# Kernel optimization log

Hardware: AMD Instinct MI355X
Metric: run time of the kernel (lower is better)

Reference implementation:

```python
import jax, jax.numpy as jnp
import numpy as np

D = 256
HEADS = 8
LEVELS = 4
POINTS = 4
HD = D // HEADS  # 32
SHAPES = [(96, 96), (48, 48), (24, 24), (12, 12)]
N_BATCH = 2


def setup_inputs() -> dict:
    key = jax.random.key(0)
    ks = jax.random.split(key, 10)
    Lin = sum(h * w for h, w in SHAPES)  # 12240
    src = jax.random.normal(ks[0], (N_BATCH, Lin, D), jnp.float32)
    reference_points = jax.random.uniform(ks[1], (N_BATCH, Lin, LEVELS, 2), jnp.float32)
    spatial_shapes = np.array(SHAPES, dtype=np.int64)
    level_start_index = np.concatenate([[0], np.cumsum([h * w for h, w in SHAPES])[:-1]]).astype(np.int64)
    s = 0.02
    w_value = s * jax.random.normal(ks[2], (D, D), jnp.float32)
    b_value = jnp.zeros((D,), jnp.float32)
    w_off = s * jax.random.normal(ks[3], (D, HEADS * LEVELS * POINTS * 2), jnp.float32)
    b_off = 0.5 * jax.random.normal(ks[4], (HEADS * LEVELS * POINTS * 2,), jnp.float32)
    w_attn = s * jax.random.normal(ks[5], (D, HEADS * LEVELS * POINTS), jnp.float32)
    b_attn = jnp.zeros((HEADS * LEVELS * POINTS,), jnp.float32)
    w_out = s * jax.random.normal(ks[6], (D, D), jnp.float32)
    b_out = jnp.zeros((D,), jnp.float32)
    gamma = jnp.ones((D,), jnp.float32)
    beta = jnp.zeros((D,), jnp.float32)
    return dict(src=src, reference_points=reference_points, spatial_shapes=spatial_shapes,
                level_start_index=level_start_index, w_value=w_value, b_value=b_value,
                w_off=w_off, b_off=b_off, w_attn=w_attn, b_attn=b_attn,
                w_out=w_out, b_out=b_out, gamma=gamma, beta=beta)


def _bilinear_sample(value_flat, H, W, loc):
    # value_flat: (N, heads, H*W, hd); loc: (N, heads, Lq, P, 2) normalized [0,1]
    # Equivalent to F.grid_sample(bilinear, padding_mode='zeros', align_corners=False)
    x = loc[..., 0] * W - 0.5
    y = loc[..., 1] * H - 0.5
    x0 = jnp.floor(x)
    y0 = jnp.floor(y)
    lx = x - x0
    ly = y - y0
    n, h, Lq, P = x.shape
    out = jnp.zeros((n, h, Lq, P, value_flat.shape[-1]), value_flat.dtype)
    for dy, wy in ((0, 1.0 - ly), (1, ly)):
        for dx, wx in ((0, 1.0 - lx), (1, lx)):
            xi = x0 + dx
            yi = y0 + dy
            valid = (xi >= 0) & (xi < W) & (yi >= 0) & (yi < H)
            idx = (jnp.clip(yi, 0, H - 1) * W + jnp.clip(xi, 0, W - 1)).astype(jnp.int32)
            v = jnp.take_along_axis(value_flat, idx.reshape(n, h, Lq * P, 1), axis=2)
            v = v.reshape(n, h, Lq, P, -1)
            out = out + v * (wx * wy * valid.astype(value_flat.dtype))[..., None]
    return out


def reference(src, reference_points, spatial_shapes, level_start_index,
              w_value, b_value, w_off, b_off, w_attn, b_attn, w_out, b_out, gamma, beta):
    N, Lq, _ = src.shape
    shapes = np.asarray(spatial_shapes)
    starts = np.asarray(level_start_index)

    # projections
    value = (src @ w_value + b_value).reshape(N, Lq, HEADS, HD)
    offsets = (src @ w_off + b_off).reshape(N, Lq, HEADS, LEVELS, POINTS, 2)
    attn = (src @ w_attn + b_attn).reshape(N, Lq, HEADS, LEVELS * POINTS)
    attn = jax.nn.softmax(attn, axis=-1).reshape(N, Lq, HEADS, LEVELS, POINTS)

    # sampling locations: ref + offset / (W_l, H_l)
    normalizer = jnp.asarray(shapes[:, ::-1].copy(), jnp.float32)  # (L, 2) = (W, H)
    loc = reference_points[:, :, None, :, None, :] + offsets / normalizer[None, None, None, :, None, :]

    out = jnp.zeros((N, HEADS, Lq, HD), src.dtype)
    for l in range(LEVELS):
        H, W = int(shapes[l, 0]), int(shapes[l, 1])
        s0 = int(starts[l])
        v_l = value[:, s0:s0 + H * W].transpose(0, 2, 1, 3)        # (N, heads, HW, hd)
        loc_l = loc[:, :, :, l].transpose(0, 2, 1, 3, 4)           # (N, heads, Lq, P, 2)
        sampled = _bilinear_sample(v_l, H, W, loc_l)               # (N, heads, Lq, P, hd)
        w_l = attn[:, :, :, l].transpose(0, 2, 1, 3)               # (N, heads, Lq, P)
        out = out + (sampled * w_l[..., None]).sum(axis=3)
    out = out.transpose(0, 2, 1, 3).reshape(N, Lq, D)
    out = out @ w_out + b_out

    # residual (dropout in eval = identity) + LayerNorm
    x = src + out
    mu = x.mean(-1, keepdims=True)
    var = x.var(-1, keepdims=True)
    return (x - mu) / jnp.sqrt(var + 1e-5) * gamma + beta
```

## Files before the change

kernel.cpp:

```cpp
#include <hip/hip_runtime.h>
#include <cstdint>
#include <cstddef>

#define D 256
#define HEADS 8
#define HD 32
#define NB 2
#define LQ 12240
#define NQ (NB * LQ)
#define PLANE (LQ * HD)

typedef __attribute__((ext_vector_type(8))) short bf16x8;
typedef __attribute__((ext_vector_type(4))) float f32x4;
typedef __bf16 bf16x2 __attribute__((ext_vector_type(2)));

__device__ __forceinline__ ushort f2bf(float f) {
    union { float f; uint32_t u; } c; c.f = f;
    uint32_t u = c.u;
    uint32_t r = (u + 0x7fffu + ((u >> 16) & 1u)) >> 16;
    return (ushort)r;
}
__device__ __forceinline__ float bflo(uint32_t u) { return __uint_as_float(u << 16); }
__device__ __forceinline__ float bfhi(uint32_t u) { return __uint_as_float(u & 0xffff0000u); }

__device__ __forceinline__ float dot2bf(uint32_t a, uint32_t b, float c) {
#if __has_builtin(__builtin_amdgcn_fdot2_f32_bf16)
    return __builtin_amdgcn_fdot2_f32_bf16(__builtin_bit_cast(bf16x2, a),
                                           __builtin_bit_cast(bf16x2, b), c, false);
#else
    return c + bflo(a) * bflo(b) + bfhi(a) * bfhi(b);
#endif
}

__global__ __launch_bounds__(256) void conv_kernel(
    const float* __restrict__ w_value, const float* __restrict__ w_off,
    const float* __restrict__ w_attn,  const float* __restrict__ b_value,
    const float* __restrict__ b_off,   const float* __restrict__ b_attn,
    const float* __restrict__ w_out,   const float* __restrict__ src,
    ushort* __restrict__ B_pack, ushort* __restrict__ w_out_t,
    float* __restrict__ b_pack, ushort* __restrict__ src_bf)
{
    const int b = blockIdx.x, k = threadIdx.x;
    if (b >= 899) {
        const size_t i = ((size_t)(b - 899) * 256 + k) * 4;
        float4 v = *(const float4*)(src + i);
        ushort4 o;
        o.x = f2bf(v.x); o.y = f2bf(v.y); o.z = f2bf(v.z); o.w = f2bf(v.w);
        *(ushort4*)(src_bf + i) = o;
        return;
    }
    if (b < 640) {
        float v;
        if (b < 256)      v = w_value[(size_t)k * 256 + b];
        else if (b < 512) v = w_off[(size_t)k * 256 + (b - 256)];
        else              v = w_attn[(size_t)k * 128 + (b - 512)];
        B_pack[(size_t)b * 256 + k] = f2bf(v);
    } else if (b < 896) {
        int n = b - 640;
        w_out_t[(size_t)n * 256 + k] = f2bf(w_out[(size_t)k * 256 + n]);
    } else if (b == 896) {
        b_pack[k] = b_value[k];
    } else if (b == 897) {
        b_pack[256 + k] = b_off[k];
    } else {
        if (k < 128) b_pack[512 + k] = b_attn[k];
    }
}

__global__ __launch_bounds__(256, 2) void proj_gemm(
    const ushort* __restrict__ src_bf, const ushort* __restrict__ B_pack,
    const float* __restrict__ b_pack,
    ushort* __restrict__ val_t, float* __restrict__ off_raw,
    float* __restrict__ attn_raw)
{
    const int tid = threadIdx.x;
    const int wv = tid >> 6, lane = tid & 63;
    const int quad = lane >> 4, ln = lane & 15;
    const int mc = blockIdx.x;
    const int by = blockIdx.y;

    const ushort* bp = B_pack + (size_t)(by * 64 + ln) * 256 + quad * 8;
    bf16x8 bfr[4][8];
#pragma unroll
    for (int t = 0; t < 4; ++t)
#pragma unroll
        for (int s = 0; s < 8; ++s)
            bfr[t][s] = *(const bf16x8*)(bp + (size_t)t * (16 * 256) + s * 32);

    float bias[4];
#pragma unroll
    for (int t = 0; t < 4; ++t) bias[t] = b_pack[by * 64 + t * 16 + ln];

    for (int i = 0; i < 3; ++i) {
        const int base = (mc * 3 + i) * 64;
        if (base >= NQ) break;
        const int row_a = base + wv * 16 + ln;
        const bool va = row_a < NQ;
        const ushort* ap = src_bf + (size_t)row_a * 256 + quad * 8;

        bf16x8 af[8];
#pragma unroll
        for (int s = 0; s < 8; ++s) {
            bf16x8 v = {0, 0, 0, 0, 0, 0, 0, 0};
            if (va) v = *(const bf16x8*)(ap + s * 32);
            af[s] = v;
        }

        f32x4 acc[4] = {{0,0,0,0},{0,0,0,0},{0,0,0,0},{0,0,0,0}};
#pragma unroll
        for (int s = 0; s < 8; ++s)
#pragma unroll
            for (int t = 0; t < 4; ++t)
                acc[t] = __builtin_amdgcn_mfma_f32_16x16x32_bf16(af[s], bfr[t][s], acc[t], 0, 0, 0);

        if (by < 4) {
#pragma unroll
            for (int t = 0; t < 4; ++t) {
                const int n_g = by * 64 + t * 16 + ln;
                const int h = n_g >> 5, hd = n_g & 31;
#pragma unroll
                for (int reg = 0; reg < 4; ++reg) {
                    int row = base + wv * 16 + quad * 4 + reg;
                    if (row < NQ) {
                        int nb = row >= LQ; int ql = row - nb * LQ;
                        val_t[(((size_t)(nb * 8 + h)) * LQ + ql) * 32 + hd] =
                            f2bf(acc[t][reg] + bias[t]);
                    }
                }
            }
        } else if (by < 8) {
#pragma unroll
            for (int t = 0; t < 4; ++t) {
                const int col = (by - 4) * 64 + t * 16 + ln;
#pragma unroll
                for (int reg = 0; reg < 4; ++reg) {
                    int row = base + wv * 16 + quad * 4 + reg;
                    if (row < NQ)
                        off_raw[(size_t)row * 256 + col] = acc[t][reg] + bias[t];
                }
            }
        } else {
#pragma unroll
            for (int t = 0; t < 4; ++t) {
                const int col = (by - 8) * 64 + t * 16 + ln;
#pragma unroll
                for (int reg = 0; reg < 4; ++reg) {
                    int row = base + wv * 16 + quad * 4 + reg;
                    if (row < NQ)
                        attn_raw[(size_t)row * 128 + col] = acc[t][reg] + bias[t];
                }
            }
        }
    }
}

__global__ __launch_bounds__(256) void pair_kernel(
    const ushort* __restrict__ val_t, uint32_t* __restrict__ val_pair)
{
    const uint32_t j = blockIdx.x * 256 + threadIdx.x;
    const uint32_t c4 = (j & 7u) * 4u;
    const uint32_t rest = j >> 3;
    const uint32_t plane = rest / LQ;
    const uint32_t pos = rest - plane * LQ;
    int l = (pos >= 9216) + (pos >= 11520) + (pos >= 12096);
    uint32_t s0 = (l > 0 ? 9216u : 0u) + (l > 1 ? 2304u : 0u) + (l > 2 ? 576u : 0u);
    uint32_t Wi = 96u >> l;
    uint32_t p = pos - s0;
    uint32_t q = (p / 3u) >> (5 - l);
    uint32_t xr = p - q * Wi;
    uint32_t nxt = (xr == Wi - 1u) ? pos : pos + 1u;
    const ushort* base = val_t + (size_t)plane * PLANE;
    uint2 lo = *(const uint2*)(base + pos * 32 + c4);
    uint2 hi = *(const uint2*)(base + nxt * 32 + c4);
    uint4 o;
    o.x = (lo.x & 0x0000ffffu) | (hi.x << 16);
    o.y = (lo.x >> 16)         | (hi.x & 0xffff0000u);
    o.z = (lo.y & 0x0000ffffu) | (hi.y << 16);
    o.w = (lo.y >> 16)         | (hi.y & 0xffff0000u);
    *(uint4*)(val_pair + ((size_t)rest * 32 + c4)) = o;
}

__global__ __launch_bounds__(256) void sample_kernel(
    const float* __restrict__ ref_pts,
    const uint32_t* __restrict__ val_pair,
    const float* __restrict__ off_raw,
    const float* attn_raw,
    uint32_t* sampled)
{
    __shared__ uint32_t sm_i[16][2][18];
    __shared__ uint32_t sm_w[16][2][18];
    const int gl = threadIdx.x >> 4;
    const int ln = threadIdx.x & 15;
    const int h     = blockIdx.x & 7;
    const int chunk = blockIdx.x >> 3;
    const int qg = chunk * 16 + gl;
    const int n  = (qg >= LQ) ? 1 : 0;
    const int l  = ln >> 2;

    float a = attn_raw[(size_t)qg * 128 + h * 16 + ln];
    float m = a;
#pragma unroll
    for (int s = 8; s; s >>= 1) m = fmaxf(m, __shfl_xor(m, s, 16));
    float e = __expf(a - m);
    float ssum = e;
#pragma unroll
    for (int s = 8; s; s >>= 1) ssum += __shfl_xor(ssum, s, 16);
    float aw = e * __builtin_amdgcn_rcpf(ssum);

    float ox = off_raw[(size_t)qg * 256 + h * 32 + ln * 2 + 0];
    float oy = off_raw[(size_t)qg * 256 + h * 32 + ln * 2 + 1];
    float rx = ref_pts[(qg * 4 + l) * 2 + 0];
    float ry = ref_pts[(qg * 4 + l) * 2 + 1];

    const int Wi = 96 >> l;
    const int Hi = Wi;
    const int s0 = (l > 0 ? 9216 : 0) + (l > 1 ? 2304 : 0) + (l > 2 ? 576 : 0);
    const float Wf = (float)Wi, Hf = (float)Hi;

    float x = fmaf(rx, Wf, ox) - 0.5f;
    float y = fmaf(ry, Hf, oy) - 0.5f;
    float x0f = floorf(x), y0f = floorf(y);
    float lx = x - x0f, ly = y - y0f;
    int x0 = (int)x0f, y0 = (int)y0f;

    float wy0 = (y0 >= 0 && y0 < Hi) ? (1.f - ly) : 0.f;
    float wy1 = (y0 + 1 >= 0 && y0 + 1 < Hi) ? ly : 0.f;
    int yc0 = min(max(y0, 0), Hi - 1);
    int yc1 = min(max(y0 + 1, 0), Hi - 1);
    float wl = (x0 >= 0 && x0 < Wi) ? (1.f - lx) : 0.f;
    float wh = (x0 + 1 >= 0 && x0 + 1 < Wi) ? lx : 0.f;
    float pl, ph;
    int xe;
    if (x0 < 0) { pl = wh; ph = 0.f; xe = x0 + 1; }
    else        { pl = wl; ph = wh;  xe = x0; }
    int xc = min(max(xe, 0), Wi - 1);
    pl *= aw; ph *= aw;

    sm_i[gl][0][ln] = (uint32_t)(s0 + yc0 * Wi + xc) * 32u;
    sm_i[gl][1][ln] = (uint32_t)(s0 + yc1 * Wi + xc) * 32u;
    sm_w[gl][0][ln] = ((uint32_t)f2bf(ph * wy0) << 16) | (uint32_t)f2bf(pl * wy0);
    sm_w[gl][1][ln] = ((uint32_t)f2bf(ph * wy1) << 16) | (uint32_t)f2bf(pl * wy1);

    const int half = ln >> 3;
    const int cb   = (ln & 7) * 4;
    const uint32_t* plane =
        val_pair + (size_t)(n * HEADS + h) * PLANE + cb;

    float a0 = 0.f, a1 = 0.f, a2 = 0.f, a3 = 0.f;
#pragma unroll
    for (int c = 0; c < 2; ++c) {
        uint4    rv[8];
        uint32_t wpk[8];
#pragma unroll
        for (int p = 0; p < 8; ++p) {
            uint32_t off = sm_i[gl][half][c * 8 + p];
            rv[p]  = *(const uint4*)(plane + off);
            wpk[p] = sm_w[gl][half][c * 8 + p];
        }
#pragma unroll
        for (int p = 0; p < 8; ++p) {
            a0 = dot2bf(rv[p].x, wpk[p], a0);
            a1 = dot2bf(rv[p].y, wpk[p], a1);
            a2 = dot2bf(rv[p].z, wpk[p], a2);
            a3 = dot2bf(rv[p].w, wpk[p], a3);
        }
    }
    a0 += __shfl_xor(a0, 8, 16);
    a1 += __shfl_xor(a1, 8, 16);
    a2 += __shfl_xor(a2, 8, 16);
    a3 += __shfl_xor(a3, 8, 16);
    if (ln < 8) {
        uint2 rr;
        rr.x = ((uint32_t)f2bf(a1) << 16) | (uint32_t)f2bf(a0);
        rr.y = ((uint32_t)f2bf(a3) << 16) | (uint32_t)f2bf(a2);
        *(uint2*)(sampled + (size_t)qg * 128 + h * 16 + 2 * ln) = rr;
    }
}

__global__ __launch_bounds__(256, 2) void out_ln_gemm(
    const ushort* __restrict__ sampled, const ushort* __restrict__ w_out_t,
    const float* __restrict__ b_out,    const float* __restrict__ src,
    const float* __restrict__ gamma,    const float* __restrict__ beta,
    float* __restrict__ out)
{
    __shared__ float sm[2][4][16][2];
    const int tid = threadIdx.x;
    const int wv = tid >> 6, lane = tid & 63;
    const int quad = lane >> 4, ln = lane & 15;

    const ushort* bp = w_out_t + (size_t)(wv * 64 + ln) * 256 + quad * 8;
    bf16x8 bfr[4][8];
#pragma unroll
    for (int t = 0; t < 4; ++t)
#pragma unroll
        for (int s = 0; s < 8; ++s)
            bfr[t][s] = *(const bf16x8*)(bp + (size_t)t * (16 * 256) + s * 32);

    float bias[4], gam[4], bet[4];
#pragma unroll
    for (int t = 0; t < 4; ++t) {
        const int col = wv * 64 + t * 16 + ln;
        bias[t] = b_out[col];
        gam[t]  = gamma[col];
        bet[t]  = beta[col];
    }

    int base = blockIdx.x * 48;

    bf16x8 af[8];
    {
        const ushort* ap = sampled + (size_t)(base + ln) * 256 + quad * 8;
#pragma unroll
        for (int s = 0; s < 8; ++s) af[s] = *(const bf16x8*)(ap + s * 32);
    }

    for (int i = 0; i < 3; ++i) {
        bf16x8 afn[8];
        if (i < 2) {
            const ushort* apn = sampled + (size_t)(base + 16 + ln) * 256 + quad * 8;
#pragma unroll
            for (int s = 0; s < 8; ++s) afn[s] = *(const bf16x8*)(apn + s * 32);
        }
        float sv[4][4];
#pragma unroll
        for (int reg = 0; reg < 4; ++reg) {
            const float* sp = src + (size_t)(base + quad * 4 + reg) * 256 + wv * 64 + ln;
#pragma unroll
            for (int t = 0; t < 4; ++t) sv[reg][t] = sp[t * 16];
        }

        f32x4 acc[4] = {{0,0,0,0},{0,0,0,0},{0,0,0,0},{0,0,0,0}};
#pragma unroll
        for (int s = 0; s < 8; ++s)
#pragma unroll
            for (int t = 0; t < 4; ++t)
                acc[t] = __builtin_amdgcn_mfma_f32_16x16x32_bf16(af[s], bfr[t][s], acc[t], 0, 0, 0);

#pragma unroll
        for (int reg = 0; reg < 4; ++reg) {
            float s1 = 0.f, s2 = 0.f;
#pragma unroll
            for (int t = 0; t < 4; ++t) {
                float v = acc[t][reg] + bias[t] + sv[reg][t];
                acc[t][reg] = v;
                s1 += v; s2 += v * v;
            }
#pragma unroll
            for (int o = 8; o; o >>= 1) {
                s1 += __shfl_xor(s1, o, 16);
                s2 += __shfl_xor(s2, o, 16);
            }
            if (ln == 0) {
                sm[i & 1][wv][quad * 4 + reg][0] = s1;
                sm[i & 1][wv][quad * 4 + reg][1] = s2;
            }
        }
        __syncthreads();

#pragma unroll
        for (int reg = 0; reg < 4; ++reg) {
            const int r16 = quad * 4 + reg;
            float s1 = sm[i & 1][0][r16][0] + sm[i & 1][1][r16][0]
                     + sm[i & 1][2][r16][0] + sm[i & 1][3][r16][0];
            float s2 = sm[i & 1][0][r16][1] + sm[i & 1][1][r16][1]
                     + sm[i & 1][2][r16][1] + sm[i & 1][3][r16][1];
            float mu  = s1 * (1.f / 256.f);
            float var = s2 * (1.f / 256.f) - mu * mu;
            float rs  = rsqrtf(var + 1e-5f);
            const int row = base + quad * 4 + reg;
            float* op = out + (size_t)row * 256 + wv * 64 + ln;
#pragma unroll
            for (int t = 0; t < 4; ++t)
                op[t * 16] = (acc[t][reg] - mu) * rs * gam[t] + bet[t];
        }

        base += 16;
#pragma unroll
        for (int s = 0; s < 8; ++s) af[s] = afn[s];
    }
}

extern "C" void kernel_launch(void* const* d_in, const int* in_sizes, int n_in,
                              void* d_out, int out_size, void* d_ws, size_t ws_size,
                              hipStream_t stream)
{
    const float* src     = (const float*)d_in[0];
    const float* refp    = (const float*)d_in[1];
    const float* w_value = (const float*)d_in[4];
    const float* b_value = (const float*)d_in[5];
    const float* w_off   = (const float*)d_in[6];
    const float* b_off   = (const float*)d_in[7];
    const float* w_attn  = (const float*)d_in[8];
    const float* b_attn  = (const float*)d_in[9];
    const float* w_out   = (const float*)d_in[10];
    const float* b_out   = (const float*)d_in[11];
    const float* gamma   = (const float*)d_in[12];
    const float* beta    = (const float*)d_in[13];

    char* ws = (char*)d_ws;
    ushort*   val_t    = (ushort*)  (ws);
    uint32_t* val_pair = (uint32_t*)(ws + 12533760);
    ushort*   src_bf   = (ushort*)  (ws + 12533760);
    float*    off_raw  = (float*)   (ws + 37601280);
    float*    attn_raw = (float*)   (ws + 62668800);
    uint32_t* sampled  = (uint32_t*)(ws + 62668800);
    ushort*   B_pack   = (ushort*)  (ws + 75202560);
    ushort*   w_out_t  = (ushort*)  (ws + 75530240);
    float*    b_pack   = (float*)   (ws + 75661312);
    float*    out      = (float*)d_out;

    conv_kernel<<<7019, 256, 0, stream>>>(w_value, w_off, w_attn, b_value, b_off,
                                          b_attn, w_out, src, B_pack, w_out_t,
                                          b_pack, src_bf);
    proj_gemm<<<dim3(128, 10), 256, 0, stream>>>(src_bf, B_pack, b_pack, val_t,
                                                 off_raw, attn_raw);
    pair_kernel<<<6120, 256, 0, stream>>>(val_t, val_pair);
    sample_kernel<<<12240, 256, 0, stream>>>(refp, val_pair, off_raw, attn_raw,
                                             sampled);
    out_ln_gemm<<<510, 256, 0, stream>>>((const ushort*)sampled, w_out_t,
                                         b_out, src, gamma, beta, out);
}
```

Baseline: 199.4 us.

## Stage B tile in LDS and give each wave a 64x64 output tile in proj_gemm

proj_gemm used to hold the whole 64-column B slice in registers and loop over three 64-row chunks, with each wave computing a 16x64 tile. Now each block stages the 64x256 B slice in padded shared memory, and each wave computes a 64x64 tile (4x4 MFMA accumulators) over 256 rows, streaming A in K chunks. The grid shrinks from 128 to 96 blocks along M. The goal is to free the large B register file for more accumulators and more A reuse per B fragment, at the cost of LDS reads and a barrier, and with fewer blocks for a 256-CU part.

```diff
diff --git a/kernel.cpp b/kernel.cpp
--- a/kernel.cpp
+++ b/kernel.cpp
@@ -73,83 +73,102 @@
     ushort* __restrict__ val_t, float* __restrict__ off_raw,
     float* __restrict__ attn_raw)
 {
+    __shared__ ushort blds[64 * 264];
     const int tid = threadIdx.x;
     const int wv = tid >> 6, lane = tid & 63;
     const int quad = lane >> 4, ln = lane & 15;
     const int mc = blockIdx.x;
     const int by = blockIdx.y;
 
-    const ushort* bp = B_pack + (size_t)(by * 64 + ln) * 256 + quad * 8;
-    bf16x8 bfr[4][8];
-#pragma unroll
-    for (int t = 0; t < 4; ++t)
-#pragma unroll
-        for (int s = 0; s < 8; ++s)
-            bfr[t][s] = *(const bf16x8*)(bp + (size_t)t * (16 * 256) + s * 32);
+#pragma unroll
+    for (int j = 0; j < 8; ++j) {
+        const int idx = j * 256 + tid;
+        const int row = idx >> 5, c16 = idx & 31;
+        *(uint4*)(blds + row * 264 + c16 * 8) =
+            *(const uint4*)(B_pack + (size_t)(by * 64 + row) * 256 + c16 * 8);
+    }
 
     float bias[4];
 #pragma unroll
     for (int t = 0; t < 4; ++t) bias[t] = b_pack[by * 64 + t * 16 + ln];
 
-    for (int i = 0; i < 3; ++i) {
-        const int base = (mc * 3 + i) * 64;
-        if (base >= NQ) break;
-        const int row_a = base + wv * 16 + ln;
-        const bool va = row_a < NQ;
-        const ushort* ap = src_bf + (size_t)row_a * 256 + quad * 8;
-
-        bf16x8 af[8];
-#pragma unroll
-        for (int s = 0; s < 8; ++s) {
+    const int rowbase = mc * 256 + wv * 64;
+    bool va[4];
+#pragma unroll
+    for (int rt = 0; rt < 4; ++rt) va[rt] = (rowbase + rt * 16 + ln) < NQ;
+
+    __syncthreads();
+
+    f32x4 acc[4][4];
+#pragma unroll
+    for (int rt = 0; rt < 4; ++rt)
+#pragma unroll
+        for (int t = 0; t < 4; ++t) acc[rt][t] = (f32x4){0.f, 0.f, 0.f, 0.f};
+
+#pragma unroll 2
+    for (int kc = 0; kc < 8; ++kc) {
+        bf16x8 af[4], bf[4];
+#pragma unroll
+        for (int rt = 0; rt < 4; ++rt) {
             bf16x8 v = {0, 0, 0, 0, 0, 0, 0, 0};
-            if (va) v = *(const bf16x8*)(ap + s * 32);
-            af[s] = v;
-        }
-
-        f32x4 acc[4] = {{0,0,0,0},{0,0,0,0},{0,0,0,0},{0,0,0,0}};
-#pragma unroll
-        for (int s = 0; s < 8; ++s)
+            if (va[rt])
+                v = *(const bf16x8*)(src_bf +
+                      (size_t)(rowbase + rt * 16 + ln) * 256 + kc * 32 + quad * 8);
+            af[rt] = v;
+        }
+#pragma unroll
+        for (int t = 0; t < 4; ++t)
+            bf[t] = *(const bf16x8*)(blds + (t * 16 + ln) * 264 + kc * 32 + quad * 8);
+#pragma unroll
+        for (int rt = 0; rt < 4; ++rt)
 #pragma unroll
             for (int t = 0; t < 4; ++t)
-                acc[t] = __builtin_amdgcn_mfma_f32_16x16x32_bf16(af[s], bfr[t][s], acc[t], 0, 0, 0);
-
-        if (by < 4) {
-#pragma unroll
-            for (int t = 0; t < 4; ++t) {
-                const int n_g = by * 64 + t * 16 + ln;
-                const int h = n_g >> 5, hd = n_g & 31;
+                acc[rt][t] = __builtin_amdgcn_mfma_f32_16x16x32_bf16(
+                                 af[rt], bf[t], acc[rt][t], 0, 0, 0);
+    }
+
+    if (by < 4) {
+#pragma unroll
+        for (int t = 0; t < 4; ++t) {
+            const int n_g = by * 64 + t * 16 + ln;
+            const int h = n_g >> 5, hd = n_g & 31;
+#pragma unroll
+            for (int rt = 0; rt < 4; ++rt)
 #pragma unroll
                 for (int reg = 0; reg < 4; ++reg) {
-                    int row = base + wv * 16 + quad * 4 + reg;
+                    const int row = rowbase + rt * 16 + quad * 4 + reg;
                     if (row < NQ) {
-                        int nb = row >= LQ; int ql = row - nb * LQ;
+                        const int nb = row >= LQ; const int ql = row - nb * LQ;
                         val_t[(((size_t)(nb * 8 + h)) * LQ + ql) * 32 + hd] =
-                            f2bf(acc[t][reg] + bias[t]);
+                            f2bf(acc[rt][t][reg] + bias[t]);
                     }
                 }
-            }
-        } else if (by < 8) {
-#pragma unroll
-            for (int t = 0; t < 4; ++t) {
-                const int col = (by - 4) * 64 + t * 16 + ln;
+        }
+    } else if (by < 8) {
+#pragma unroll
+        for (int t = 0; t < 4; ++t) {
+            const int col = (by - 4) * 64 + t * 16 + ln;
+#pragma unroll
+            for (int rt = 0; rt < 4; ++rt)
 #pragma unroll
                 for (int reg = 0; reg < 4; ++reg) {
-                    int row = base + wv * 16 + quad * 4 + reg;
+                    const int row = rowbase + rt * 16 + quad * 4 + reg;
                     if (row < NQ)
-                        off_raw[(size_t)row * 256 + col] = acc[t][reg] + bias[t];
+                        off_raw[(size_t)row * 256 + col] = acc[rt][t][reg] + bias[t];
                 }
-            }
-        } else {
-#pragma unroll
-            for (int t = 0; t < 4; ++t) {
-                const int col = (by - 8) * 64 + t * 16 + ln;
+        }
+    } else {
+#pragma unroll
+        for (int t = 0; t < 4; ++t) {
+            const int col = (by - 8) * 64 + t * 16 + ln;
+#pragma unroll
+            for (int rt = 0; rt < 4; ++rt)
 #pragma unroll
                 for (int reg = 0; reg < 4; ++reg) {
-                    int row = base + wv * 16 + quad * 4 + reg;
+                    const int row = rowbase + rt * 16 + quad * 4 + reg;
                     if (row < NQ)
-                        attn_raw[(size_t)row * 128 + col] = acc[t][reg] + bias[t];
+                        attn_raw[(size_t)row * 128 + col] = acc[rt][t][reg] + bias[t];
                 }
-            }
         }
     }
 }
@@ -412,8 +431,8 @@
     conv_kernel<<<7019, 256, 0, stream>>>(w_value, w_off, w_attn, b_value, b_off,
                                           b_attn, w_out, src, B_pack, w_out_t,
                                           b_pack, src_bf);
-    proj_gemm<<<dim3(128, 10), 256, 0, stream>>>(src_bf, B_pack, b_pack, val_t,
-                                                 off_raw, attn_raw);
+    proj_gemm<<<dim3(96, 10), 256, 0, stream>>>(src_bf, B_pack, b_pack, val_t,
+                                                off_raw, attn_raw);
     pair_kernel<<<6120, 256, 0, stream>>>(val_t, val_pair);
     sample_kernel<<<12240, 256, 0, stream>>>(refp, val_pair, off_raw, attn_raw,
                                              sampled);
```

New measurement: 184.5 us. -7.5%, faster.
